# Optimization experiments

Measured on AMD Instinct MI355X. Metric: run time of the kernel, lower is better.

Reference implementation:

```python
import jax, jax.numpy as jnp
import numpy as np

IN_FEATURES = 3
MAPPING_SIZE = 128
FF_SCALE = 10.0
HIDDEN = 512
HIDDEN_LAYERS = 5
OUT_FEATURES = 3
OMEGA0 = 30.0
TWO_PI = 2.0 * np.pi


def setup_inputs() -> dict:
    key = jax.random.key(0)
    ks = jax.random.split(key, 10)
    B, L = 1, 262144
    coords = jax.random.uniform(ks[0], (B, L, IN_FEATURES), jnp.float32, -1.0, 1.0)
    # Fourier feature projection (random Gaussian buffer, scale=10)
    B_ff = jax.random.normal(ks[1], (IN_FEATURES, MAPPING_SIZE), jnp.float32) * FF_SCALE
    ff_dim = 2 * MAPPING_SIZE  # 256
    # First sine layer: is_first=True -> U(-1/in, 1/in)
    W_first = jax.random.uniform(ks[2], (HIDDEN, ff_dim), jnp.float32, -1.0 / ff_dim, 1.0 / ff_dim)
    b_first = jax.random.uniform(ks[3], (HIDDEN,), jnp.float32, -1.0 / np.sqrt(ff_dim), 1.0 / np.sqrt(ff_dim))
    # Hidden sine layers: U(-sqrt(6/in)/omega0, +)
    wh = np.sqrt(6.0 / HIDDEN) / OMEGA0
    W_hidden = jax.random.uniform(ks[4], (HIDDEN_LAYERS, HIDDEN, HIDDEN), jnp.float32, -wh, wh)
    b_hidden = jax.random.uniform(ks[5], (HIDDEN_LAYERS, HIDDEN), jnp.float32, -1.0 / np.sqrt(HIDDEN), 1.0 / np.sqrt(HIDDEN))
    # Final linear: U(-sqrt(6/hidden)/omega0, +)
    W_out = jax.random.uniform(ks[6], (OUT_FEATURES, HIDDEN), jnp.float32, -wh, wh)
    b_out = jax.random.uniform(ks[7], (OUT_FEATURES,), jnp.float32, -1.0 / np.sqrt(HIDDEN), 1.0 / np.sqrt(HIDDEN))
    return {"coords": coords, "B_ff": B_ff, "W_first": W_first, "b_first": b_first,
            "W_hidden": W_hidden, "b_hidden": b_hidden, "W_out": W_out, "b_out": b_out}


def reference(coords, B_ff, W_first, b_first, W_hidden, b_hidden, W_out, b_out):
    # Fourier feature encoding: [B,L,3] -> [B,L,256]
    proj = TWO_PI * (coords @ B_ff)
    h = jnp.concatenate([jnp.sin(proj), jnp.cos(proj)], axis=-1)
    # First sine layer
    h = jnp.sin(OMEGA0 * (jnp.einsum('bli,oi->blo', h, W_first) + b_first))
    # Hidden sine layers (stacked weights, scanned)
    def step(h, wb):
        w, b = wb
        return jnp.sin(OMEGA0 * (jnp.einsum('bli,oi->blo', h, w) + b)), None
    h, _ = jax.lax.scan(step, h, (W_hidden, b_hidden))
    # Outermost linear
    return jnp.einsum('bli,oi->blo', h, W_out) + b_out
```

## Files before the change

kernel.cpp:

```cpp
#include <hip/hip_runtime.h>


#define L_TOTAL 262144
#define TOK 128
#define THREADS 512
#define C_SC 4.77464829275686f

typedef _Float16 f16x8 __attribute__((ext_vector_type(8)));
typedef _Float16 f16x4 __attribute__((ext_vector_type(4)));
typedef float    f32x4 __attribute__((ext_vector_type(4)));

#define N1 (512 * 256)
#define N2 (N1 + 5 * 512 * 512)
#define N3 (N2 + 16 * 512)
#define NBIAS 3072

__global__ void convert_weights(const float* __restrict__ Wf,
                                const float* __restrict__ Wh,
                                const float* __restrict__ Wo,
                                const float* __restrict__ bf,
                                const float* __restrict__ bh,
                                _Float16* __restrict__ o,
                                float* __restrict__ biasC) {
  int i = blockIdx.x * blockDim.x + threadIdx.x;
  if (i < N3) {
    float v;
    if (i < N1) {
      const int blk = i >> 9, w = i & 511;
      const int lane = w >> 3, e = w & 7;
      const int mt = blk >> 3, ks = blk & 7;
      const int row = mt * 16 + (lane & 15);
      const int col = ks * 32 + (lane >> 4) * 8 + e;
      v = Wf[row * 256 + col];
    } else if (i < N2) {
      int j = i - N1;
      const int l = j >> 18;
      j &= (1 << 18) - 1;
      const int blk = j >> 9, w = j & 511;
      const int lane = w >> 3, e = w & 7;
      const int mt = blk >> 4, ks = blk & 15;
      const int row = mt * 16 + (lane & 15);
      const int col = ks * 32 + (lane >> 4) * 8 + e;
      v = Wh[l * (512 * 512) + row * 512 + col];
    } else {
      const int r = (i - N2) >> 9, c = (i - N2) & 511;
      v = (r < 3) ? Wo[r * 512 + c] : 0.0f;
    }
    o[i] = (_Float16)v;
  } else if (i < N3 + NBIAS) {
    int j = i - N3;
    biasC[j] = (j < 512 ? bf[j] : bh[j - 512]) * C_SC;
  }
}

__device__ __forceinline__ int h_elem(int chunk, int token) {
  return (chunk * 128 + token) * 8;
}

template <int K>
__device__ __forceinline__ void sine_layer(const _Float16* __restrict__ W,
                                           const float* __restrict__ biasC,
                                           _Float16* hb, int lane, int lr,
                                           int lg, int m0) {
  constexpr int KS = K / 32;
  f32x4 acc[4][8];
#pragma unroll
  for (int mt = 0; mt < 4; ++mt)
#pragma unroll
    for (int nt = 0; nt < 8; ++nt)
      acc[mt][nt] = (f32x4){0.f, 0.f, 0.f, 0.f};

  const _Float16* wb[4];
#pragma unroll
  for (int mt = 0; mt < 4; ++mt)
    wb[mt] = &W[(((m0 >> 4) + mt) * KS) * 512 + lane * 8];

  f16x8 a[3][4], b[2][8];
#pragma unroll
  for (int mt = 0; mt < 4; ++mt) a[0][mt] = *(const f16x8*)(wb[mt]);
#pragma unroll
  for (int mt = 0; mt < 4; ++mt) a[1][mt] = *(const f16x8*)(wb[mt] + 512);
#pragma unroll
  for (int nt = 0; nt < 8; ++nt)
    b[0][nt] = *(const f16x8*)&hb[h_elem(lg, nt * 16 + lr)];

#pragma unroll
  for (int ks = 0; ks < KS; ++ks) {
    const int cur = ks & 1;
    const int ai = ks % 3;
    if (ks + 1 < KS) {
#pragma unroll
      for (int nt = 0; nt < 8; ++nt)
        b[cur ^ 1][nt] =
            *(const f16x8*)&hb[h_elem((ks + 1) * 4 + lg, nt * 16 + lr)];
    }
    if (ks + 2 < KS) {
#pragma unroll
      for (int mt = 0; mt < 4; ++mt)
        a[(ks + 2) % 3][mt] = *(const f16x8*)(wb[mt] + (ks + 2) * 512);
    }
#pragma unroll
    for (int mt = 0; mt < 4; ++mt)
#pragma unroll
      for (int nt = 0; nt < 8; ++nt)
        acc[mt][nt] = __builtin_amdgcn_mfma_f32_16x16x32_f16(
            a[ai][mt], b[cur][nt], acc[mt][nt], 0, 0, 0);
  }
  __syncthreads();

#pragma unroll
  for (int mt = 0; mt < 4; ++mt) {
    const int ob = m0 + mt * 16 + lg * 4;
    const f32x4 bb = *(const f32x4*)&biasC[ob];
    const int wbase = (ob >> 3) * 128 * 8 + (ob & 7);
#pragma unroll
    for (int nt = 0; nt < 8; ++nt) {
      f16x4 hv;
#pragma unroll
      for (int r = 0; r < 4; ++r) {
        float pre = fmaf(acc[mt][nt][r], C_SC, bb[r]);
        hv[r] = (_Float16)__builtin_amdgcn_sinf(pre);
      }
      *(f16x4*)&hb[wbase + (nt * 16 + lr) * 8] = hv;
    }
  }
  __syncthreads();
}

__global__ __launch_bounds__(THREADS, 2) void siren_kernel(
    const float* __restrict__ coords, const float* __restrict__ bff,
    const float* __restrict__ biasC, const float* __restrict__ b_out,
    const _Float16* __restrict__ wf, const _Float16* __restrict__ wh,
    const _Float16* __restrict__ wo, float* __restrict__ out) {
  extern __shared__ _Float16 hb[];
  const int tid = threadIdx.x;
  const int t0 = blockIdx.x * TOK;

  if ((tid >> 6) < 4) __builtin_amdgcn_s_setprio(1);

  {
    const int t = tid & 127;
    const int q = tid >> 7;
    const float c0 = coords[(t0 + t) * 3 + 0];
    const float c1 = coords[(t0 + t) * 3 + 1];
    const float c2 = coords[(t0 + t) * 3 + 2];
#pragma unroll
    for (int cb = 0; cb < 4; ++cb) {
      f16x8 sv, cv;
#pragma unroll
      for (int e = 0; e < 8; ++e) {
        const int j = q * 32 + cb * 8 + e;
        float r = fmaf(c0, bff[j], fmaf(c1, bff[128 + j], c2 * bff[256 + j]));
        sv[e] = (_Float16)__builtin_amdgcn_sinf(r);
        cv[e] = (_Float16)__builtin_amdgcn_cosf(r);
      }
      *(f16x8*)&hb[h_elem(q * 4 + cb, t)] = sv;
      *(f16x8*)&hb[h_elem(16 + q * 4 + cb, t)] = cv;
    }
  }
  __syncthreads();

  const int lane = tid & 63;
  const int lr = lane & 15;
  const int lg = lane >> 4;
  const int m0 = (tid >> 6) * 64;

  sine_layer<256>(wf, biasC, hb, lane, lr, lg, m0);
#pragma unroll 1
  for (int l = 0; l < 5; ++l)
    sine_layer<512>(wh + l * (512 * 512), biasC + 512 + l * 512, hb, lane, lr,
                    lg, m0);

  {
    const int wave = tid >> 6;
    f32x4 acc = {0.f, 0.f, 0.f, 0.f};
#pragma unroll
    for (int ks = 0; ks < 16; ++ks) {
      f16x8 a = *(const f16x8*)&wo[lr * 512 + ks * 32 + lg * 8];
      f16x8 b = *(const f16x8*)&hb[h_elem(ks * 4 + lg, wave * 16 + lr)];
      acc = __builtin_amdgcn_mfma_f32_16x16x32_f16(a, b, acc, 0, 0, 0);
    }
    if (lg == 0) {
      const int t = t0 + wave * 16 + lr;
      out[t * 3 + 0] = acc[0] + b_out[0];
      out[t * 3 + 1] = acc[1] + b_out[1];
      out[t * 3 + 2] = acc[2] + b_out[2];
    }
  }
}

extern "C" void kernel_launch(void* const* d_in, const int* in_sizes, int n_in,
                              void* d_out, int out_size, void* d_ws,
                              size_t ws_size, hipStream_t stream) {
  const float* coords = (const float*)d_in[0];
  const float* bff    = (const float*)d_in[1];
  const float* Wf     = (const float*)d_in[2];
  const float* bf     = (const float*)d_in[3];
  const float* Wh     = (const float*)d_in[4];
  const float* bh     = (const float*)d_in[5];
  const float* Wo     = (const float*)d_in[6];
  const float* bo     = (const float*)d_in[7];
  float* out = (float*)d_out;

  _Float16* w16 = (_Float16*)d_ws;
  float* biasC = (float*)(w16 + N3);

  convert_weights<<<(N3 + NBIAS + 255) / 256, 256, 0, stream>>>(
      Wf, Wh, Wo, bf, bh, w16, biasC);

  const size_t lds_bytes = 64 * 128 * 8 * sizeof(_Float16);
  siren_kernel<<<L_TOTAL / TOK, THREADS, lds_bytes, stream>>>(
      coords, bff, biasC, bo, w16, w16 + N1, w16 + N2, out);
}
```

Before: 753.1 us.

## Prefetch next layer's weights and bias during epilogue; fold scale into weights

Pre-multiplies the first and hidden weights by the omega scale constant at conversion time. The accumulators are initialised with the scaled bias, so the epilogue only applies sin with no fma. The next layer's first two weight k-slices and its bias are loaded before the sine/store epilogue of the current layer, hiding global-load latency at each layer boundary. Scaling the fp16 weights slightly changes rounding, and carrying the prefetched registers across layers may raise register pressure.

```diff
diff --git a/kernel.cpp b/kernel.cpp
--- a/kernel.cpp
+++ b/kernel.cpp
@@ -31,7 +31,7 @@
       const int mt = blk >> 3, ks = blk & 7;
       const int row = mt * 16 + (lane & 15);
       const int col = ks * 32 + (lane >> 4) * 8 + e;
-      v = Wf[row * 256 + col];
+      v = Wf[row * 256 + col] * C_SC;
     } else if (i < N2) {
       int j = i - N1;
       const int l = j >> 18;
@@ -41,7 +41,7 @@
       const int mt = blk >> 4, ks = blk & 15;
       const int row = mt * 16 + (lane & 15);
       const int col = ks * 32 + (lane >> 4) * 8 + e;
-      v = Wh[l * (512 * 512) + row * 512 + col];
+      v = Wh[l * (512 * 512) + row * 512 + col] * C_SC;
     } else {
       const int r = (i - N2) >> 9, c = (i - N2) & 511;
       v = (r < 3) ? Wo[r * 512 + c] : 0.0f;
@@ -57,29 +57,25 @@
   return (chunk * 128 + token) * 8;
 }
 
-template <int K>
-__device__ __forceinline__ void sine_layer(const _Float16* __restrict__ W,
-                                           const float* __restrict__ biasC,
-                                           _Float16* hb, int lane, int lr,
-                                           int lg, int m0) {
+template <int K, int KN>
+__device__ __forceinline__ void sine_layer(
+    const _Float16* __restrict__ W, const _Float16* __restrict__ Wnext,
+    const float* __restrict__ biasNext, _Float16* hb, f16x8 (&a)[3][4],
+    f32x4 (&bb)[4], int lane, int lr, int lg, int m0) {
   constexpr int KS = K / 32;
   f32x4 acc[4][8];
 #pragma unroll
   for (int mt = 0; mt < 4; ++mt)
 #pragma unroll
     for (int nt = 0; nt < 8; ++nt)
-      acc[mt][nt] = (f32x4){0.f, 0.f, 0.f, 0.f};
+      acc[mt][nt] = bb[mt];
 
   const _Float16* wb[4];
 #pragma unroll
   for (int mt = 0; mt < 4; ++mt)
     wb[mt] = &W[(((m0 >> 4) + mt) * KS) * 512 + lane * 8];
 
-  f16x8 a[3][4], b[2][8];
-#pragma unroll
-  for (int mt = 0; mt < 4; ++mt) a[0][mt] = *(const f16x8*)(wb[mt]);
-#pragma unroll
-  for (int mt = 0; mt < 4; ++mt) a[1][mt] = *(const f16x8*)(wb[mt] + 512);
+  f16x8 b[2][8];
 #pragma unroll
   for (int nt = 0; nt < 8; ++nt)
     b[0][nt] = *(const f16x8*)&hb[h_elem(lg, nt * 16 + lr)];
@@ -108,18 +104,26 @@
   }
   __syncthreads();
 
+  if constexpr (KN > 0) {
+#pragma unroll
+    for (int mt = 0; mt < 4; ++mt) {
+      const _Float16* p = &Wnext[(((m0 >> 4) + mt) * KN) * 512 + lane * 8];
+      a[0][mt] = *(const f16x8*)p;
+      a[1][mt] = *(const f16x8*)(p + 512);
+      bb[mt] = *(const f32x4*)&biasNext[m0 + mt * 16 + lg * 4];
+    }
+  }
+
 #pragma unroll
   for (int mt = 0; mt < 4; ++mt) {
     const int ob = m0 + mt * 16 + lg * 4;
-    const f32x4 bb = *(const f32x4*)&biasC[ob];
     const int wbase = (ob >> 3) * 128 * 8 + (ob & 7);
 #pragma unroll
     for (int nt = 0; nt < 8; ++nt) {
       f16x4 hv;
 #pragma unroll
       for (int r = 0; r < 4; ++r) {
-        float pre = fmaf(acc[mt][nt][r], C_SC, bb[r]);
-        hv[r] = (_Float16)__builtin_amdgcn_sinf(pre);
+        hv[r] = (_Float16)__builtin_amdgcn_sinf(acc[mt][nt][r]);
       }
       *(f16x4*)&hb[wbase + (nt * 16 + lr) * 8] = hv;
     }
@@ -138,6 +142,22 @@
 
   if ((tid >> 6) < 4) __builtin_amdgcn_s_setprio(1);
 
+  const int lane = tid & 63;
+  const int lr = lane & 15;
+  const int lg = lane >> 4;
+  const int wave = tid >> 6;
+  const int m0 = wave * 64;
+
+  f16x8 a[3][4];
+  f32x4 bb[4];
+#pragma unroll
+  for (int mt = 0; mt < 4; ++mt) {
+    const _Float16* p = &wf[(((m0 >> 4) + mt) * 8) * 512 + lane * 8];
+    a[0][mt] = *(const f16x8*)p;
+    a[1][mt] = *(const f16x8*)(p + 512);
+    bb[mt] = *(const f32x4*)&biasC[m0 + mt * 16 + lg * 4];
+  }
+
   {
     const int t = tid & 127;
     const int q = tid >> 7;
@@ -160,25 +180,22 @@
   }
   __syncthreads();
 
-  const int lane = tid & 63;
-  const int lr = lane & 15;
-  const int lg = lane >> 4;
-  const int m0 = (tid >> 6) * 64;
-
-  sine_layer<256>(wf, biasC, hb, lane, lr, lg, m0);
+  sine_layer<256, 16>(wf, wh, biasC + 512, hb, a, bb, lane, lr, lg, m0);
 #pragma unroll 1
-  for (int l = 0; l < 5; ++l)
-    sine_layer<512>(wh + l * (512 * 512), biasC + 512 + l * 512, hb, lane, lr,
-                    lg, m0);
+  for (int l = 0; l < 4; ++l)
+    sine_layer<512, 16>(wh + l * (512 * 512), wh + (l + 1) * (512 * 512),
+                        biasC + 512 + (l + 1) * 512, hb, a, bb, lane, lr, lg,
+                        m0);
+  sine_layer<512, 0>(wh + 4 * (512 * 512), nullptr, nullptr, hb, a, bb, lane,
+                     lr, lg, m0);
 
   {
-    const int wave = tid >> 6;
     f32x4 acc = {0.f, 0.f, 0.f, 0.f};
 #pragma unroll
     for (int ks = 0; ks < 16; ++ks) {
-      f16x8 a = *(const f16x8*)&wo[lr * 512 + ks * 32 + lg * 8];
-      f16x8 b = *(const f16x8*)&hb[h_elem(ks * 4 + lg, wave * 16 + lr)];
-      acc = __builtin_amdgcn_mfma_f32_16x16x32_f16(a, b, acc, 0, 0, 0);
+      f16x8 av = *(const f16x8*)&wo[lr * 512 + ks * 32 + lg * 8];
+      f16x8 bv = *(const f16x8*)&hb[h_elem(ks * 4 + lg, wave * 16 + lr)];
+      acc = __builtin_amdgcn_mfma_f32_16x16x32_f16(av, bv, acc, 0, 0, 0);
     }
     if (lg == 0) {
       const int t = t0 + wave * 16 + lr;
```

After: 1.002 ms. +33.0%, slower.
